# Performance work log

Hardware: AMD Instinct MI355X
Metric: run time of the kernel (lower is better)

The kernel has to match this reference:

```python
import jax, jax.numpy as jnp
import numpy as np

B, H, W = 2, 512, 512


def _conv(x, w, b):
    y = jax.lax.conv_general_dilated(
        x, w, window_strides=(1, 1), padding='SAME',
        dimension_numbers=('NCHW', 'OIHW', 'NCHW'))
    return y + b[None, :, None, None]


def _pool(x):
    return jax.lax.reduce_window(x, -jnp.inf, jax.lax.max,
                                 (1, 1, 2, 2), (1, 1, 2, 2), 'VALID')


def _vgg_pools(x, ws, bs):
    # vgg16.features up to modules 4, 9, 16 (the first three maxpools)
    r = jax.nn.relu
    x = r(_conv(x, ws[0], bs[0]))
    x = r(_conv(x, ws[1], bs[1]))
    p1 = _pool(x)                      # [B,64,256,256]  (module 4)
    x = r(_conv(p1, ws[2], bs[2]))
    x = r(_conv(x, ws[3], bs[3]))
    p2 = _pool(x)                      # [B,128,128,128] (module 9)
    x = r(_conv(p2, ws[4], bs[4]))
    x = r(_conv(x, ws[5], bs[5]))
    x = r(_conv(x, ws[6], bs[6]))
    p3 = _pool(x)                      # [B,256,64,64]   (module 16)
    return (p1, p2, p3)


def _style(a, g):
    # faithful to per-(b,c) torch.mm(phi.T, phi): WxW Gram per channel
    Bc, C, Hc, Wc = a.shape
    Kp = 1.0 / (C * Hc * Wc)
    Ga = jnp.einsum('bchw,bchv->bcwv', a, a)
    Gg = jnp.einsum('bchw,bchv->bcwv', g, g)
    return jnp.sum(jnp.abs(Kp * (Ga - Gg))) / (C * C)


def setup_inputs() -> dict:
    key = jax.random.key(0)
    ks = jax.random.split(key, 20)
    igt = jax.random.normal(ks[0], (B, 3, H, W), dtype=jnp.float32)
    iout = jax.random.normal(ks[1], (B, 3, H, W), dtype=jnp.float32)
    mask = jax.random.randint(ks[2], (B, 1, H, W), 0, 2).astype(jnp.float32)
    # VGG16 conv stack up to features[16]: channel plan per torchvision vgg16
    chans = [(3, 64), (64, 64), (64, 128), (128, 128), (128, 256), (256, 256), (256, 256)]
    inp = {'igt': igt, 'iout': iout, 'mask': mask}
    for i, (cin, cout) in enumerate(chans):
        scale = np.sqrt(2.0 / (cin * 9)).astype(np.float32)
        inp[f'w{i}'] = jax.random.normal(ks[3 + i], (cout, cin, 3, 3), dtype=jnp.float32) * scale
        inp[f'b{i}'] = jnp.zeros((cout,), dtype=jnp.float32)
    return inp


def reference(igt, iout, mask, w0, b0, w1, b1, w2, b2, w3, b3, w4, b4, w5, b5, w6, b6):
    ws = (w0, w1, w2, w3, w4, w5, w6)
    bs = (b0, b1, b2, b3, b4, b5, b6)
    m = jnp.where(mask != 0, 1.0, 0.0).astype(igt.dtype)   # mask[mask!=0]=1
    icomp = jnp.where(m == 1, igt, iout)                   # make_comp (broadcast over C)
    Bn = igt.shape[0]
    N = 3 * H * W * Bn
    diff = iout - igt
    # l_hole: original loops B times over the FULL norm -> factor B (faithful)
    l_hole = Bn * jnp.sum(jnp.abs((1.0 - m) * diff)) / N
    # l_valid: per-sample norms summed == full L1
    l_valid = jnp.sum(jnp.abs(m * diff)) / N
    pool_out = _vgg_pools(iout, ws, bs)
    pool_gt = _vgg_pools(igt, ws, bs)
    pool_comp = _vgg_pools(icomp, ws, bs)
    # l_perc: original always normalizes by prod(pool_gt[0].shape) (faithful bug)
    Nigt = float(np.prod(pool_gt[0].shape))
    l_perc = 0.0
    for i in range(3):
        l_perc = l_perc + (jnp.sum(jnp.abs(pool_out[i] - pool_gt[i]))
                           + jnp.sum(jnp.abs(pool_comp[i] - pool_gt[i]))) / Nigt
    l_style_comp = sum(_style(pool_comp[i], pool_gt[i]) for i in range(3))
    l_style_out = sum(_style(pool_out[i], pool_gt[i]) for i in range(3))
    return l_hole + l_valid + l_perc + l_style_comp + l_style_out
```

## Files before the change

kernel.cpp:

```cpp
#include <hip/hip_runtime.h>
#include <hip/hip_bf16.h>


typedef __attribute__((ext_vector_type(8))) short bf16x8_t;
typedef __attribute__((ext_vector_type(4))) float f32x4_t;
typedef __attribute__((ext_vector_type(16))) float f32x16_t;
typedef __attribute__((ext_vector_type(8))) int i32x8_t;
typedef __attribute__((ext_vector_type(4))) short s16x4_t;

typedef const __attribute__((address_space(1))) void* gas_t;
typedef __attribute__((address_space(3))) void* las_t;

__device__ __forceinline__ void gld16(const void* g, void* l) {
  __builtin_amdgcn_global_load_lds((gas_t)g, (las_t)l, 16, 0, 0);
}

__device__ __forceinline__ unsigned char f2fp8(float v) {
  return (unsigned char)(__builtin_amdgcn_cvt_pk_fp8_f32(v, v, 0, false) & 0xff);
}

__device__ __forceinline__ i32x8_t ld_frag(const unsigned char* lds, int row,
                                           int h) {
  const int sw = (row >> 1) & 3;
  const unsigned char* base = lds + row * 64;
  uint4 lo = *(const uint4*)(base + (((2 * h) ^ sw) << 4));
  uint4 hi = *(const uint4*)(base + (((2 * h + 1) ^ sw) << 4));
  i32x8_t r;
  r[0] = lo.x; r[1] = lo.y; r[2] = lo.z; r[3] = lo.w;
  r[4] = hi.x; r[5] = hi.y; r[6] = hi.z; r[7] = hi.w;
  return r;
}

__device__ __forceinline__ i32x8_t ld32g(const unsigned char* p) {
  uint4 lo = *(const uint4*)p;
  uint4 hi = *(const uint4*)(p + 16);
  i32x8_t r;
  r[0] = lo.x; r[1] = lo.y; r[2] = lo.z; r[3] = lo.w;
  r[4] = hi.x; r[5] = hi.y; r[6] = hi.z; r[7] = hi.w;
  return r;
}

__device__ __forceinline__ float blk_sum256(float v, float* s4) {
#pragma unroll
  for (int o = 32; o > 0; o >>= 1) v += __shfl_down(v, o);
  int w = threadIdx.x >> 6;
  if ((threadIdx.x & 63) == 0) s4[w] = v;
  __syncthreads();
  float r = s4[0] + s4[1] + s4[2] + s4[3];
  __syncthreads();
  return r;
}

__global__ void init_slots(float* slots) {
  if (threadIdx.x < 32) slots[threadIdx.x] = 0.0f;
}

__global__ __launch_bounds__(256) void pack_all(
    const float* __restrict__ w1, const float* __restrict__ w2,
    const float* __restrict__ w3, const float* __restrict__ w4,
    const float* __restrict__ w5, const float* __restrict__ w6,
    const float* __restrict__ w7, const float* __restrict__ igt,
    const float* __restrict__ iout, const float* __restrict__ mask,
    unsigned char* __restrict__ wpk, __hip_bfloat16* __restrict__ w1k,
    float* __restrict__ slots) {
  __shared__ float s4[4];
  const int b = blockIdx.x;
  if (b < 1692) {
    int start, Cin, Cout;
    long off;
    const float* w;
    if (b < 36)        { start = 0;    Cin = 64;  Cout = 64;  off = 0;       w = w2; }
    else if (b < 108)  { start = 36;   Cin = 64;  Cout = 128; off = 36864;   w = w3; }
    else if (b < 252)  { start = 108;  Cin = 128; Cout = 128; off = 110592;  w = w4; }
    else if (b < 540)  { start = 252;  Cin = 128; Cout = 256; off = 258048;  w = w5; }
    else if (b < 1116) { start = 540;  Cin = 256; Cout = 256; off = 552960;  w = w6; }
    else               { start = 1116; Cin = 256; Cout = 256; off = 1142784; w = w7; }
    unsigned char* wp = wpk + off;
    int i = (b - start) * 256 + threadIdx.x;
    int c4n = Cin >> 2;
    int o = i % 9;
    int rem = i / 9;
    int c4 = rem % c4n;
    int co = rem / c4n;
    int dy = o / 3, dx = o % 3;
    unsigned r = 0;
#pragma unroll
    for (int k = 0; k < 4; ++k) {
      int ci = c4 * 4 + k;
      float v = w[((co * Cin + ci) * 3 + dy) * 3 + dx];
      r |= (unsigned)f2fp8(v) << (8 * k);
    }
    *(unsigned*)(wp + ((long)(o * Cout + co)) * Cin + c4 * 4) = r;
  } else if (b < 1700) {
    int i = (b - 1692) * 256 + threadIdx.x;
    int co = i >> 5, k = i & 31;
    float v = 0.0f;
    if (k < 27) {
      int dy = k / 9, r = k - dy * 9;
      int dx = r / 3, ci = r - dx * 3;
      v = w1[((co * 3 + ci) * 3 + dy) * 3 + dx];
    }
    w1k[i] = __float2bfloat16(v);
  } else {
    int vb = b - 1700;
    float ah = 0.0f, av = 0.0f;
    for (int idx = vb * 256 + threadIdx.x; idx < 1572864; idx += 304 * 256) {
      int pix = idx & 262143;
      int n = idx / 786432;
      float mk = mask[n * 262144 + pix];
      bool m = (mk != 0.0f);
      float d = fabsf(iout[idx] - igt[idx]);
      if (m) av += d; else ah += d;
    }
    float r = blk_sum256(ah, s4);
    if (threadIdx.x == 0) atomicAdd(&slots[0], r);
    r = blk_sum256(av, s4);
    if (threadIdx.x == 0) atomicAdd(&slots[1], r);
  }
}

__global__ __launch_bounds__(256, 2) void conv1f(
    const float* __restrict__ igt, const float* __restrict__ iout,
    const float* __restrict__ mask, const __hip_bfloat16* __restrict__ wk,
    const float* __restrict__ bias, unsigned char* __restrict__ outb,
    int n0, int NB, long ystride) {
  __shared__ __align__(16) short ApS[512 * 32];
  __shared__ __align__(16) short BwS[64 * 32];
  __shared__ __align__(16) s16x4_t Sel[660];
  const int tid = threadIdx.x;
  const int lane = tid & 63;
  const int wv = tid >> 6;
  const int quad = lane >> 4, l15 = lane & 15;
  const int s = blockIdx.z / NB;
  const int nl = blockIdx.z % NB;
  const int sample = n0 + nl;
  const int x0 = blockIdx.x << 6;
  const int y0 = blockIdx.y << 3;

  if (wv < 4) gld16(wk + (lane >> 2) * 32 + (lane & 3) * 8, &BwS[wv << 9]);

  for (int hp = tid; hp < 660; hp += 256) {
    int r = hp / 66, c = hp - r * 66;
    int gy = y0 - 1 + r, gx = x0 - 1 + c;
    bool inb = (gy >= 0 && gy < 512 && gx >= 0 && gx < 512);
    int p = gy * 512 + gx;
    bool useG;
    if (s == 0) useG = true;
    else if (s == 1) useG = false;
    else useG = inb && (mask[sample * 262144 + (inb ? p : 0)] != 0.0f);
    const float* src = useG ? igt : iout;
    s16x4_t v4;
#pragma unroll
    for (int ci = 0; ci < 3; ++ci) {
      float v = inb ? src[sample * 786432 + ci * 262144 + p] : 0.0f;
      __hip_bfloat16 bv = __float2bfloat16(v);
      v4[ci] = *(short*)&bv;
    }
    v4[3] = 0;
    Sel[hp] = v4;
  }
  __syncthreads();

#pragma unroll
  for (int t = 0; t < 2; ++t) {
    int pix = tid + t * 256;
    int r = pix >> 6, c = pix & 63;
    __align__(16) __hip_bfloat16 buf[32];
#pragma unroll
    for (int k = 27; k < 32; ++k) buf[k] = __float2bfloat16(0.0f);
#pragma unroll
    for (int dy = 0; dy < 3; ++dy)
#pragma unroll
      for (int dx = 0; dx < 3; ++dx) {
        s16x4_t v4 = Sel[(r + dy) * 66 + (c + dx)];
        short* bs = (short*)buf;
        bs[dy * 9 + dx * 3 + 0] = v4[0];
        bs[dy * 9 + dx * 3 + 1] = v4[1];
        bs[dy * 9 + dx * 3 + 2] = v4[2];
      }
#pragma unroll
    for (int q = 0; q < 4; ++q)
      *(uint4*)&ApS[pix * 32 + q * 8] = *(const uint4*)&buf[q * 8];
  }
  __syncthreads();

  f32x4_t acc[8][4];
#pragma unroll
  for (int mt = 0; mt < 8; ++mt)
#pragma unroll
    for (int nt = 0; nt < 4; ++nt) acc[mt][nt] = (f32x4_t)0.0f;

  bf16x8_t bf[4];
#pragma unroll
  for (int nt = 0; nt < 4; ++nt)
    bf[nt] = *(const bf16x8_t*)&BwS[(nt * 16 + l15) * 32 + quad * 8];
#pragma unroll
  for (int mt = 0; mt < 8; ++mt) {
    const int rl = 2 * wv + (mt >> 2);
    const int pl = (mt & 3) * 16 + l15;
    const bf16x8_t a = *(const bf16x8_t*)&ApS[(rl * 64 + pl) * 32 + quad * 8];
#pragma unroll
    for (int nt = 0; nt < 4; ++nt)
      acc[mt][nt] = __builtin_amdgcn_mfma_f32_16x16x32_bf16(a, bf[nt],
                                                            acc[mt][nt], 0, 0, 0);
  }

  float bv[4];
#pragma unroll
  for (int nt = 0; nt < 4; ++nt) bv[nt] = bias[nt * 16 + l15];

  __syncthreads();
  unsigned char* O8 = (unsigned char*)ApS;
#pragma unroll
  for (int mt = 0; mt < 8; ++mt) {
    const int ry = 2 * wv + (mt >> 2);
#pragma unroll
    for (int nt = 0; nt < 4; ++nt) {
      const int col = nt * 16 + l15;
#pragma unroll
      for (int reg = 0; reg < 4; ++reg) {
        int px = (mt & 3) * 16 + quad * 4 + reg;
        float v = fmaxf(acc[mt][nt][reg] + bv[nt], 0.0f);
        O8[((ry << 6) + px) * 64 + col] = f2fp8(v);
      }
    }
  }
  __syncthreads();
  unsigned char* out = outb + (long)s * ystride;
#pragma unroll
  for (int j = 0; j < 8; ++j) {
    int L = (j * 256 + tid) << 4;
    int x = (L >> 6) & 63;
    int cq = L & 63;
    *(uint4*)(out + (((long)nl * 512 + y0 + j) * 512 + x0 + x) * 64 + cq) =
        *(const uint4*)&O8[L];
  }
}

__global__ __launch_bounds__(256, 3) void conv_f8(
    const unsigned char* __restrict__ act, const unsigned char* __restrict__ wp,
    const float* __restrict__ bias, unsigned char* __restrict__ out,
    const unsigned char* __restrict__ zp, int Cin, int Cout, int H, int W) {
  __shared__ __align__(16) unsigned char ApS[400 * 64];
  const int tid = threadIdx.x;
  const int lane = tid & 63;
  const int wv = tid >> 6;
  const int l31 = lane & 31;
  const int h = lane >> 5;
  const int pr = wv & 1;
  const int ch = wv >> 1;
  const int coB = Cout >> 6;
  const int n = blockIdx.z / coB;
  const int co0 = (blockIdx.z % coB) << 6;
  const int x0 = blockIdx.x << 6;
  const int y0 = blockIdx.y << 2;
  const int spos = lane >> 2;
  const int sc = lane & 3;

  f32x16_t acc[2][2];
#pragma unroll
  for (int dr = 0; dr < 2; ++dr)
#pragma unroll
    for (int mh = 0; mh < 2; ++mh) acc[dr][mh] = (f32x16_t)0.0f;

  for (int cb = 0; cb < Cin; cb += 64) {
    if (cb) __syncthreads();
    for (int u = wv; u < 25; u += 4) {
      int pos = (u << 4) + spos;
      int q = sc ^ ((pos >> 1) & 3);
      int r = pos / 66, c = pos - r * 66;
      int gy = y0 - 1 + r, gx = x0 - 1 + c;
      const unsigned char* src = zp;
      if (pos < 396 && gy >= 0 && gy < H && gx >= 0 && gx < W)
        src = act + ((long)((long)n * H + gy) * W + gx) * Cin + cb + (q << 4);
      gld16(src, &ApS[u << 10]);
    }
    __syncthreads();

    const unsigned char* wl =
        wp + ((long)(co0 + (ch << 5) + l31)) * Cin + cb + (h << 5);
#pragma unroll
    for (int dx = 0; dx < 3; ++dx) {
      i32x8_t Af[2][4];
#pragma unroll
      for (int mh = 0; mh < 2; ++mh)
#pragma unroll
        for (int ri = 0; ri < 4; ++ri)
          Af[mh][ri] =
              ld_frag(ApS, (2 * pr + ri) * 66 + mh * 32 + l31 + dx, h);
#pragma unroll
      for (int dy = 0; dy < 3; ++dy) {
        const int o = dy * 3 + dx;
        i32x8_t Bf = ld32g(wl + (long)o * Cout * Cin);
#pragma unroll
        for (int dr = 0; dr < 2; ++dr)
#pragma unroll
          for (int mh = 0; mh < 2; ++mh)
            acc[dr][mh] = __builtin_amdgcn_mfma_scale_f32_32x32x64_f8f6f4(
                Af[mh][dr + dy], Bf, acc[dr][mh], 0, 0, 0,
                0x7F7F7F7F, 0, 0x7F7F7F7F);
      }
    }
  }

  const float bv = bias[co0 + (ch << 5) + l31];

  __syncthreads();
#pragma unroll
  for (int dr = 0; dr < 2; ++dr) {
    const int ry = 2 * pr + dr;
#pragma unroll
    for (int mh = 0; mh < 2; ++mh) {
#pragma unroll
      for (int reg = 0; reg < 16; ++reg) {
        int rowM = (reg & 3) + 8 * (reg >> 2) + 4 * h;
        int x = mh * 32 + rowM;
        float v = fmaxf(acc[dr][mh][reg] + bv, 0.0f);
        ApS[((ry << 6) + x) * 64 + (ch << 5) + l31] = f2fp8(v);
      }
    }
  }
  __syncthreads();
#pragma unroll
  for (int j = 0; j < 4; ++j) {
    int L = (j * 256 + tid) << 4;
    int ry = L >> 12;
    int x = (L >> 6) & 63;
    int cq = L & 63;
    *(uint4*)(out + (((long)n * H + y0 + ry) * W + x0 + x) * Cout + co0 + cq) =
        *(const uint4*)&ApS[L];
  }
}

__global__ __launch_bounds__(256, 3) void conv_f8p(
    const unsigned char* __restrict__ act, const unsigned char* __restrict__ wp,
    const float* __restrict__ bias, unsigned char* __restrict__ outF,
    __hip_bfloat16* __restrict__ outB, const unsigned char* __restrict__ zp,
    int Cin, int Cout, int H, int W) {
  __shared__ __align__(16) unsigned char ApS[400 * 64];
  const int tid = threadIdx.x;
  const int lane = tid & 63;
  const int wv = tid >> 6;
  const int l31 = lane & 31;
  const int h = lane >> 5;
  const int pr = wv & 1;
  const int ch = wv >> 1;
  const int coB = Cout >> 6;
  const int n = blockIdx.z / coB;
  const int co0 = (blockIdx.z % coB) << 6;
  const int x0g = blockIdx.x << 6;
  const int y0 = blockIdx.y << 2;
  const int spos = lane >> 2;
  const int sc = lane & 3;

  f32x16_t acc[2][2];
#pragma unroll
  for (int dr = 0; dr < 2; ++dr)
#pragma unroll
    for (int mh = 0; mh < 2; ++mh) acc[dr][mh] = (f32x16_t)0.0f;

  for (int cb = 0; cb < Cin; cb += 64) {
    if (cb) __syncthreads();
    for (int u = wv; u < 25; u += 4) {
      int pos = (u << 4) + spos;
      int q = sc ^ ((pos >> 1) & 3);
      int r = pos / 66, c = pos - r * 66;
      int gy = y0 - 1 + r, gx = x0g - 1 + c;
      const unsigned char* src = zp;
      if (pos < 396 && gy >= 0 && gy < H && gx >= 0 && gx < W)
        src = act + ((long)((long)n * H + gy) * W + gx) * Cin + cb + (q << 4);
      gld16(src, &ApS[u << 10]);
    }
    __syncthreads();

    const unsigned char* wl =
        wp + ((long)(co0 + (ch << 5) + l31)) * Cin + cb + (h << 5);
#pragma unroll
    for (int dx = 0; dx < 3; ++dx) {
      i32x8_t Af[2][4];
#pragma unroll
      for (int mh = 0; mh < 2; ++mh)
#pragma unroll
        for (int ri = 0; ri < 4; ++ri)
          Af[mh][ri] =
              ld_frag(ApS, (2 * pr + ri) * 66 + mh * 32 + l31 + dx, h);
#pragma unroll
      for (int dy = 0; dy < 3; ++dy) {
        const int o = dy * 3 + dx;
        i32x8_t Bf = ld32g(wl + (long)o * Cout * Cin);
#pragma unroll
        for (int dr = 0; dr < 2; ++dr)
#pragma unroll
          for (int mh = 0; mh < 2; ++mh)
            acc[dr][mh] = __builtin_amdgcn_mfma_scale_f32_32x32x64_f8f6f4(
                Af[mh][dr + dy], Bf, acc[dr][mh], 0, 0, 0,
                0x7F7F7F7F, 0, 0x7F7F7F7F);
      }
    }
  }

  const int Ho = H >> 1, Wo = W >> 1;
  const int ho0 = blockIdx.y << 1;
  const int wo0 = blockIdx.x << 5;
  const float bv = bias[co0 + (ch << 5) + l31];

  __syncthreads();
  unsigned char* F8 = ApS;
  __hip_bfloat16* BB = (__hip_bfloat16*)(ApS + 4096);
#pragma unroll
  for (int mh = 0; mh < 2; ++mh) {
#pragma unroll
    for (int p8 = 0; p8 < 8; ++p8) {
      const int reg = 2 * p8;
      float m0 = fmaxf(fmaxf(acc[0][mh][reg], acc[0][mh][reg + 1]),
                       fmaxf(acc[1][mh][reg], acc[1][mh][reg + 1]));
      float v = fmaxf(m0 + bv, 0.0f);
      int rowM = (reg & 3) + 8 * (reg >> 2) + 4 * h;
      int wo = mh * 16 + (rowM >> 1);
      int off = ((pr * 32 + wo) << 6) + (ch << 5) + l31;
      if (outF) F8[off] = f2fp8(v);
      BB[off] = __float2bfloat16(v);
    }
  }
  __syncthreads();
  if (outF) {
    int L = tid << 4;
    int hl = L >> 11;
    int wo = (L >> 6) & 31;
    int cq = L & 63;
    *(uint4*)(outF + (((long)n * Ho + ho0 + hl) * Wo + wo0 + wo) * Cout + co0 +
              cq) = *(const uint4*)&F8[L];
  }
#pragma unroll
  for (int j = 0; j < 2; ++j) {
    int S = (j * 256 + tid) << 3;
    int hl = S >> 11;
    int wo = (S >> 6) & 31;
    int cq = S & 63;
    *(uint4*)(outB + (((long)n * Ho + ho0 + hl) * Wo + wo0 + wo) * Cout + co0 +
              cq) = *(const uint4*)&BB[S];
  }
}

__global__ __launch_bounds__(256) void transpose_k(
    const __hip_bfloat16* __restrict__ in, __hip_bfloat16* __restrict__ out,
    int C, int Ho, int Wo) {
  const int cl = threadIdx.x & 31;
  const int wl = threadIdx.x >> 5;
  const int cg = C >> 5;
  const int j = blockIdx.z / cg;
  const int c = (blockIdx.z % cg) * 32 + cl;
  const int wo = blockIdx.x * 8 + wl;
  const int ho0 = blockIdx.y * 8;
  __align__(16) __hip_bfloat16 res[8];
#pragma unroll
  for (int i = 0; i < 8; ++i)
    res[i] = in[(((long)j * Ho + ho0 + i) * Wo + wo) * C + c];
  *(uint4*)&out[((long)(j * C + c) * Wo + wo) * Ho + ho0] =
      *(const uint4*)res;
}

__global__ __launch_bounds__(256) void perc_kernel(
    const __hip_bfloat16* __restrict__ gt, const __hip_bfloat16* __restrict__ cur,
    int M8, int gN, float* __restrict__ slots) {
  __shared__ float s4[4];
  const uint4* g4 = (const uint4*)gt;
  const uint4* c4 = (const uint4*)cur;
  float acc = 0.0f;
  for (int i = blockIdx.x * 256 + threadIdx.x; i < M8; i += gridDim.x * 256) {
    int ig = (i >= gN) ? i - gN : i;
    uint4 g = g4[ig], c = c4[i];
    const unsigned* gu = (const unsigned*)&g;
    const unsigned* cu = (const unsigned*)&c;
#pragma unroll
    for (int k = 0; k < 4; ++k) {
      float g0 = __uint_as_float(gu[k] << 16);
      float g1 = __uint_as_float(gu[k] & 0xffff0000u);
      float c0 = __uint_as_float(cu[k] << 16);
      float c1 = __uint_as_float(cu[k] & 0xffff0000u);
      acc += fabsf(c0 - g0) + fabsf(c1 - g1);
    }
  }
  float r = blk_sum256(acc, s4);
  if (threadIdx.x == 0) atomicAdd(&slots[2], r);
}

template <int BM>
__global__ __launch_bounds__(256) void gram_mfma(
    const __hip_bfloat16* __restrict__ gt_p,
    const __hip_bfloat16* __restrict__ cur_p, int Wp, int Hp, int gtm,
    float fscale, float* __restrict__ slots) {
  constexpr int COLS = BM + 64;
  constexpr int WR = BM / 4;
  constexpr int MT = WR / 16;
  __shared__ __align__(16) short S[2 * COLS * 40];
  __shared__ float s4[4];
  const int tid = threadIdx.x;
  const int lane = tid & 63;
  const int wvi = tid >> 6;
  const int quad = lane >> 4, l15 = lane & 15;
  const int vt = blockIdx.x * 64;
  const int wt = blockIdx.y * BM;
  const long plane = (long)blockIdx.z * Wp * Hp;
  const long plane_g = (long)(blockIdx.z % gtm) * Wp * Hp;
  const __hip_bfloat16* bases[2] = {gt_p + plane_g, cur_p + plane};

  f32x4_t acc[2][MT][4];
#pragma unroll
  for (int t = 0; t < 2; ++t)
#pragma unroll
    for (int mt = 0; mt < MT; ++mt)
#pragma unroll
      for (int nt = 0; nt < 4; ++nt) acc[t][mt][nt] = (f32x4_t)0.0f;

  const int nchunk = 2 * COLS * 4;
  for (int h0 = 0; h0 < Hp; h0 += 32) {
    for (int e = tid; e < nchunk; e += 256) {
      int chunk = e & 3;
      int colt = e >> 2;
      int t = colt / COLS;
      int col = colt - t * COLS;
      int sc = (col < BM) ? (wt + col) : (vt + col - BM);
      uint4 v = *(const uint4*)(bases[t] + (long)sc * Hp + h0 + chunk * 8);
      *(uint4*)&S[(t * COLS + col) * 40 + chunk * 8] = v;
    }
    __syncthreads();
#pragma unroll
    for (int t = 0; t < 2; ++t) {
      bf16x8_t bf[4];
#pragma unroll
      for (int nt = 0; nt < 4; ++nt)
        bf[nt] = *(const bf16x8_t*)&S[(t * COLS + BM + nt * 16 + l15) * 40 +
                                      quad * 8];
#pragma unroll
      for (int mt = 0; mt < MT; ++mt) {
        bf16x8_t a = *(const bf16x8_t*)&S[(t * COLS + wvi * WR + mt * 16 + l15) *
                                              40 + quad * 8];
#pragma unroll
        for (int nt = 0; nt < 4; ++nt)
          acc[t][mt][nt] = __builtin_amdgcn_mfma_f32_16x16x32_bf16(
              a, bf[nt], acc[t][mt][nt], 0, 0, 0);
      }
    }
    __syncthreads();
  }

  float local = 0.0f;
#pragma unroll
  for (int mt = 0; mt < MT; ++mt)
#pragma unroll
    for (int nt = 0; nt < 4; ++nt)
#pragma unroll
      for (int reg = 0; reg < 4; ++reg)
        local += fabsf(acc[1][mt][nt][reg] - acc[0][mt][nt][reg]);
  float r = blk_sum256(local, s4);
  if (tid == 0) atomicAdd(&slots[3], r * fscale);
}

__global__ void combine_kernel(const float* __restrict__ slots,
                               float* __restrict__ out) {
  if (threadIdx.x == 0) {
    const float Nn = 1572864.0f;
    const float Nigt = 8388608.0f;
    out[0] = 2.0f * slots[0] / Nn + slots[1] / Nn + slots[2] / Nigt + slots[3];
  }
}

extern "C" void kernel_launch(void* const* d_in, const int* in_sizes, int n_in,
                              void* d_out, int out_size, void* d_ws,
                              size_t ws_size, hipStream_t stream) {
  (void)in_sizes; (void)n_in; (void)out_size;
  const float* igt = (const float*)d_in[0];
  const float* iout = (const float*)d_in[1];
  const float* mask = (const float*)d_in[2];
  const float* w[7];
  const float* b[7];
  for (int i = 0; i < 7; ++i) {
    w[i] = (const float*)d_in[3 + 2 * i];
    b[i] = (const float*)d_in[4 + 2 * i];
  }
  float* slots = (float*)d_ws;
  const unsigned char* zp = (const unsigned char*)d_ws + 64;

  unsigned char* wpk = (unsigned char*)((char*)d_ws + 256);
  __hip_bfloat16* w1k = (__hip_bfloat16*)((char*)d_ws + 256 + 1732608);

  const size_t NEED2 = 194674944ULL;
  const int NB = (ws_size >= NEED2) ? 2 : 1;
  const int B3 = 3 * NB;
  const size_t M = (size_t)NB;

  char* base = (char*)d_ws + 1736960;
  unsigned char* P1N8 = (unsigned char*)base;
  __hip_bfloat16* P2T = (__hip_bfloat16*)base;
  char* Y1base = base + M * 16777216;
  unsigned char* Y1 = (unsigned char*)Y1base;
  __hip_bfloat16* pgT1 = (__hip_bfloat16*)Y1base;
  __hip_bfloat16* pcT1 = (__hip_bfloat16*)(Y1base + M * 8388608);
  unsigned char* P2N8 = (unsigned char*)(Y1base + M * 25165824);
  __hip_bfloat16* P2Nb = (__hip_bfloat16*)(Y1base + M * 31457280);
  __hip_bfloat16* P3Nb = (__hip_bfloat16*)Y1base;
  __hip_bfloat16* P3T = (__hip_bfloat16*)(Y1base + M * 6291456);
  char* Cbase = base + M * 67108864;
  __hip_bfloat16* P1Nb = (__hip_bfloat16*)Cbase;
  unsigned char* T = (unsigned char*)Cbase;
  unsigned char* Y5 = (unsigned char*)Cbase;
  unsigned char* Y6 = (unsigned char*)(Cbase + M * 12582912);

  const float fs1 = (float)(1.0 / (4194304.0 * 4096.0));
  const float fs2 = (float)(1.0 / (2097152.0 * 16384.0));
  const float fs3 = (float)(1.0 / (1048576.0 * 65536.0));

  init_slots<<<1, 64, 0, stream>>>(slots);
  pack_all<<<2004, 256, 0, stream>>>(w[0], w[1], w[2], w[3], w[4], w[5], w[6],
                                     igt, iout, mask, wpk, w1k, slots);

  for (int n0 = 0; n0 < 2; n0 += NB) {
    conv1f<<<dim3(8, 64, 3 * NB), 256, 0, stream>>>(
        igt, iout, mask, w1k, b[0], Y1, n0, NB, (long)(M * 16777216));
    conv_f8p<<<dim3(8, 128, 3 * NB), 256, 0, stream>>>(
        Y1, wpk + 0, b[1], P1N8, P1Nb, zp, 64, 64, 512, 512);
    transpose_k<<<dim3(32, 32, 3 * NB * 2), 256, 0, stream>>>(P1Nb, pgT1, 64,
                                                              256, 256);
    perc_kernel<<<304, 256, 0, stream>>>(pgT1, pcT1, NB * 1048576,
                                         NB * 524288, slots);
    gram_mfma<128><<<dim3(4, 2, NB * 128), 256, 0, stream>>>(
        pgT1, pcT1, 256, 256, NB * 64, fs1, slots);

    conv_f8<<<dim3(4, 64, B3 * 2), 256, 0, stream>>>(
        P1N8, wpk + 36864, b[2], T, zp, 64, 128, 256, 256);
    conv_f8p<<<dim3(4, 64, B3 * 2), 256, 0, stream>>>(
        T, wpk + 110592, b[3], P2N8, P2Nb, zp, 128, 128, 256, 256);
    transpose_k<<<dim3(16, 16, B3 * 4), 256, 0, stream>>>(P2Nb, P2T, 128, 128,
                                                          128);
    perc_kernel<<<304, 256, 0, stream>>>(P2T, P2T + M * 2097152, NB * 524288,
                                         NB * 262144, slots);
    gram_mfma<128><<<dim3(2, 1, NB * 256), 256, 0, stream>>>(
        P2T, P2T + M * 2097152, 128, 128, NB * 128, fs2, slots);

    conv_f8<<<dim3(2, 32, B3 * 4), 256, 0, stream>>>(
        P2N8, wpk + 258048, b[4], Y5, zp, 128, 256, 128, 128);
    conv_f8<<<dim3(2, 32, B3 * 4), 256, 0, stream>>>(
        Y5, wpk + 552960, b[5], Y6, zp, 256, 256, 128, 128);
    conv_f8p<<<dim3(2, 32, B3 * 4), 256, 0, stream>>>(
        Y6, wpk + 1142784, b[6], (unsigned char*)nullptr, P3Nb, zp, 256, 256,
        128, 128);
    transpose_k<<<dim3(8, 8, B3 * 8), 256, 0, stream>>>(P3Nb, P3T, 256, 64, 64);
    perc_kernel<<<304, 256, 0, stream>>>(P3T, P3T + M * 1048576, NB * 262144,
                                         NB * 131072, slots);
    gram_mfma<64><<<dim3(1, 1, NB * 512), 256, 0, stream>>>(
        P3T, P3T + M * 1048576, 64, 64, NB * 256, fs3, slots);
  }

  combine_kernel<<<1, 64, 0, stream>>>(slots, (float*)d_out);
}
```

Baseline: 685.5 us.

## Double-buffer LDS activation tiles in fp8 conv kernels to overlap loads with MFMA

Both fp8 conv kernels now keep two LDS activation buffers and issue the global_load_lds for the next 64-channel block before computing on the current one. One barrier per iteration replaces the previous pair. LDS use per block doubles to about 50KB, which may lower how many blocks fit per CU below the three requested in launch bounds. The epilogue reuses the last-used buffer, and the trailing barrier in the loop keeps that reuse safe.

Measured after the change: 727.3 us. 6.1% more time.

```diff
diff --git a/kernel.cpp b/kernel.cpp
--- a/kernel.cpp
+++ b/kernel.cpp
@@ -241,7 +241,7 @@
     const unsigned char* __restrict__ act, const unsigned char* __restrict__ wp,
     const float* __restrict__ bias, unsigned char* __restrict__ out,
     const unsigned char* __restrict__ zp, int Cin, int Cout, int H, int W) {
-  __shared__ __align__(16) unsigned char ApS[400 * 64];
+  __shared__ __align__(16) unsigned char ApS[2][25 * 1024];
   const int tid = threadIdx.x;
   const int lane = tid & 63;
   const int wv = tid >> 6;
@@ -256,15 +256,11 @@
   const int y0 = blockIdx.y << 2;
   const int spos = lane >> 2;
   const int sc = lane & 3;
-
-  f32x16_t acc[2][2];
-#pragma unroll
-  for (int dr = 0; dr < 2; ++dr)
-#pragma unroll
-    for (int mh = 0; mh < 2; ++mh) acc[dr][mh] = (f32x16_t)0.0f;
-
-  for (int cb = 0; cb < Cin; cb += 64) {
-    if (cb) __syncthreads();
+  const int CB = Cin >> 6;
+
+  auto STAGE = [&](int cbi) {
+    unsigned char* dst = ApS[cbi & 1];
+    const int cb = cbi << 6;
     for (int u = wv; u < 25; u += 4) {
       int pos = (u << 4) + spos;
       int q = sc ^ ((pos >> 1) & 3);
@@ -273,10 +269,22 @@
       const unsigned char* src = zp;
       if (pos < 396 && gy >= 0 && gy < H && gx >= 0 && gx < W)
         src = act + ((long)((long)n * H + gy) * W + gx) * Cin + cb + (q << 4);
-      gld16(src, &ApS[u << 10]);
-    }
-    __syncthreads();
-
+      gld16(src, dst + (u << 10));
+    }
+  };
+
+  f32x16_t acc[2][2];
+#pragma unroll
+  for (int dr = 0; dr < 2; ++dr)
+#pragma unroll
+    for (int mh = 0; mh < 2; ++mh) acc[dr][mh] = (f32x16_t)0.0f;
+
+  STAGE(0);
+  __syncthreads();
+  for (int cbi = 0; cbi < CB; ++cbi) {
+    if (cbi + 1 < CB) STAGE(cbi + 1);
+    const unsigned char* A = ApS[cbi & 1];
+    const int cb = cbi << 6;
     const unsigned char* wl =
         wp + ((long)(co0 + (ch << 5) + l31)) * Cin + cb + (h << 5);
 #pragma unroll
@@ -286,8 +294,7 @@
       for (int mh = 0; mh < 2; ++mh)
 #pragma unroll
         for (int ri = 0; ri < 4; ++ri)
-          Af[mh][ri] =
-              ld_frag(ApS, (2 * pr + ri) * 66 + mh * 32 + l31 + dx, h);
+          Af[mh][ri] = ld_frag(A, (2 * pr + ri) * 66 + mh * 32 + l31 + dx, h);
 #pragma unroll
       for (int dy = 0; dy < 3; ++dy) {
         const int o = dy * 3 + dx;
@@ -301,11 +308,12 @@
                 0x7F7F7F7F, 0, 0x7F7F7F7F);
       }
     }
+    __syncthreads();
   }
 
   const float bv = bias[co0 + (ch << 5) + l31];
 
-  __syncthreads();
+  unsigned char* O8 = ApS[(CB - 1) & 1];
 #pragma unroll
   for (int dr = 0; dr < 2; ++dr) {
     const int ry = 2 * pr + dr;
@@ -316,7 +324,7 @@
         int rowM = (reg & 3) + 8 * (reg >> 2) + 4 * h;
         int x = mh * 32 + rowM;
         float v = fmaxf(acc[dr][mh][reg] + bv, 0.0f);
-        ApS[((ry << 6) + x) * 64 + (ch << 5) + l31] = f2fp8(v);
+        O8[((ry << 6) + x) * 64 + (ch << 5) + l31] = f2fp8(v);
       }
     }
   }
@@ -328,7 +336,7 @@
     int x = (L >> 6) & 63;
     int cq = L & 63;
     *(uint4*)(out + (((long)n * H + y0 + ry) * W + x0 + x) * Cout + co0 + cq) =
-        *(const uint4*)&ApS[L];
+        *(const uint4*)&O8[L];
   }
 }
 
@@ -337,7 +345,7 @@
     const float* __restrict__ bias, unsigned char* __restrict__ outF,
     __hip_bfloat16* __restrict__ outB, const unsigned char* __restrict__ zp,
     int Cin, int Cout, int H, int W) {
-  __shared__ __align__(16) unsigned char ApS[400 * 64];
+  __shared__ __align__(16) unsigned char ApS[2][25 * 1024];
   const int tid = threadIdx.x;
   const int lane = tid & 63;
   const int wv = tid >> 6;
@@ -352,15 +360,11 @@
   const int y0 = blockIdx.y << 2;
   const int spos = lane >> 2;
   const int sc = lane & 3;
-
-  f32x16_t acc[2][2];
-#pragma unroll
-  for (int dr = 0; dr < 2; ++dr)
-#pragma unroll
-    for (int mh = 0; mh < 2; ++mh) acc[dr][mh] = (f32x16_t)0.0f;
-
-  for (int cb = 0; cb < Cin; cb += 64) {
-    if (cb) __syncthreads();
+  const int CB = Cin >> 6;
+
+  auto STAGE = [&](int cbi) {
+    unsigned char* dst = ApS[cbi & 1];
+    const int cb = cbi << 6;
     for (int u = wv; u < 25; u += 4) {
       int pos = (u << 4) + spos;
       int q = sc ^ ((pos >> 1) & 3);
@@ -369,10 +373,22 @@
       const unsigned char* src = zp;
       if (pos < 396 && gy >= 0 && gy < H && gx >= 0 && gx < W)
         src = act + ((long)((long)n * H + gy) * W + gx) * Cin + cb + (q << 4);
-      gld16(src, &ApS[u << 10]);
-    }
-    __syncthreads();
-
+      gld16(src, dst + (u << 10));
+    }
+  };
+
+  f32x16_t acc[2][2];
+#pragma unroll
+  for (int dr = 0; dr < 2; ++dr)
+#pragma unroll
+    for (int mh = 0; mh < 2; ++mh) acc[dr][mh] = (f32x16_t)0.0f;
+
+  STAGE(0);
+  __syncthreads();
+  for (int cbi = 0; cbi < CB; ++cbi) {
+    if (cbi + 1 < CB) STAGE(cbi + 1);
+    const unsigned char* A = ApS[cbi & 1];
+    const int cb = cbi << 6;
     const unsigned char* wl =
         wp + ((long)(co0 + (ch << 5) + l31)) * Cin + cb + (h << 5);
 #pragma unroll
@@ -382,8 +398,7 @@
       for (int mh = 0; mh < 2; ++mh)
 #pragma unroll
         for (int ri = 0; ri < 4; ++ri)
-          Af[mh][ri] =
-              ld_frag(ApS, (2 * pr + ri) * 66 + mh * 32 + l31 + dx, h);
+          Af[mh][ri] = ld_frag(A, (2 * pr + ri) * 66 + mh * 32 + l31 + dx, h);
 #pragma unroll
       for (int dy = 0; dy < 3; ++dy) {
         const int o = dy * 3 + dx;
@@ -397,6 +412,7 @@
                 0x7F7F7F7F, 0, 0x7F7F7F7F);
       }
     }
+    __syncthreads();
   }
 
   const int Ho = H >> 1, Wo = W >> 1;
@@ -404,9 +420,8 @@
   const int wo0 = blockIdx.x << 5;
   const float bv = bias[co0 + (ch << 5) + l31];
 
-  __syncthreads();
-  unsigned char* F8 = ApS;
-  __hip_bfloat16* BB = (__hip_bfloat16*)(ApS + 4096);
+  unsigned char* F8 = ApS[(CB - 1) & 1];
+  __hip_bfloat16* BB = (__hip_bfloat16*)(F8 + 4096);
 #pragma unroll
   for (int mh = 0; mh < 2; ++mh) {
 #pragma unroll
```
